# Kernel optimization log

Hardware: AMD Instinct MI355X
Metric: run time of the kernel (lower is better)

Reference implementation:

```python
import jax, jax.numpy as jnp
import numpy as np

B, T, C = 2, 4096, 768
H = 12
D = C // H  # head_dim = 64
SCALE = np.sqrt(D).astype(np.float32)


def setup_inputs() -> dict:
    key = jax.random.key(0)
    ks = jax.random.split(key, 5)
    s = 0.02
    return {
        "x": jax.random.normal(ks[0], (B, T, C), dtype=jnp.float32),
        "Wqkv": jax.random.normal(ks[1], (C, 3 * C), dtype=jnp.float32) * s,
        "bqkv": jnp.zeros((3 * C,), dtype=jnp.float32),
        "Wout": jax.random.normal(ks[2], (C, C), dtype=jnp.float32) * s,
        "bout": jnp.zeros((C,), dtype=jnp.float32),
    }


def reference(x, Wqkv, bqkv, Wout, bout):
    Bx, Tx, Cx = x.shape
    qkv = x @ Wqkv + bqkv                                   # [B,T,3C]
    qkv = qkv.reshape(Bx, Tx, 3, H, D)
    q, k, v = [jnp.moveaxis(qkv[:, :, i], 2, 1) for i in range(3)]  # each [B,H,T,D]
    attn = jnp.einsum("bhqd,bhkd->bhqk", q, k) / SCALE      # [B,H,T,T]
    causal = jnp.tril(jnp.ones((Tx, Tx), dtype=bool))
    attn = jnp.where(causal, attn, jnp.float32(-jnp.inf))
    attn = jax.nn.softmax(attn, axis=-1)
    out = jnp.einsum("bhqk,bhkd->bhqd", attn, v)            # [B,H,T,D]
    out = jnp.moveaxis(out, 1, 2).reshape(Bx, Tx, Cx)       # [B,T,C]
    return out @ Wout + bout
```

## Files before the change

kernel.cpp:

```cpp
#include <hip/hip_runtime.h>
#include <hip/hip_bf16.h>

#define T_DIM 4096
#define H_N 12
#define D_H 64
#define C_DIM 768
#define B_N 2

typedef short bf16x8 __attribute__((ext_vector_type(8)));
typedef float f32x4 __attribute__((ext_vector_type(4)));

__device__ __forceinline__ short f2bf(float f) {
    union { float f; unsigned u; } x; x.f = f;
    unsigned r = x.u + 0x7fffu + ((x.u >> 16) & 1u);
    return (short)(r >> 16);
}
__device__ __forceinline__ unsigned pk2bf(float a, float b) {
    union { float f; unsigned u; } x, y; x.f = a; y.f = b;
    unsigned ua = x.u + 0x7fffu + ((x.u >> 16) & 1u);
    unsigned ub = y.u + 0x7fffu + ((y.u >> 16) & 1u);
    return (ua >> 16) | (ub & 0xffff0000u);
}
__device__ __forceinline__ unsigned pktrunc(float lo, float hi) {
    union { float f; unsigned u; } a, b; a.f = lo; b.f = hi;
    return __builtin_amdgcn_perm(b.u, a.u, 0x07060302u);
}
__device__ __forceinline__ float bf2f(short s) {
    union { unsigned u; float f; } x; x.u = ((unsigned)(unsigned short)s) << 16;
    return x.f;
}

__device__ __forceinline__ void async_copy16(const void* g, void* l) {
    __builtin_amdgcn_global_load_lds(
        (const __attribute__((address_space(1))) unsigned*)g,
        (__attribute__((address_space(3))) unsigned*)l, 16, 0, 0);
}

#define Q_SCALE 0.18033688011112042f

__global__ __launch_bounds__(256) void xconv_kernel(
    const float* __restrict__ x, short* __restrict__ xb)
{
    size_t i = ((size_t)blockIdx.x * 256 + threadIdx.x) * 8;
    float4 a = *(const float4*)(x + i);
    float4 b = *(const float4*)(x + i + 4);
    unsigned pk[4];
    pk[0] = pk2bf(a.x, a.y); pk[1] = pk2bf(a.z, a.w);
    pk[2] = pk2bf(b.x, b.y); pk[3] = pk2bf(b.z, b.w);
    *(uint4*)(xb + i) = *(uint4*)pk;
}

__global__ __launch_bounds__(256) void wtrans_kernel(
    const float* __restrict__ W, short* __restrict__ Wt, int K, int N)
{
    const int wave = threadIdx.x >> 6, lane = threadIdx.x & 63;
    const int n = blockIdx.x * 256 + wave * 64 + lane;
    const int k0 = blockIdx.y * 128;
    for (int k = k0; k < k0 + 128; k += 8) {
        unsigned pk[4];
#pragma unroll
        for (int j = 0; j < 4; ++j)
            pk[j] = pk2bf(W[(size_t)(k + 2 * j) * N + n],
                          W[(size_t)(k + 2 * j + 1) * N + n]);
        *(uint4*)(Wt + (size_t)n * K + k) = *(uint4*)pk;
    }
}

__global__ __launch_bounds__(256) void qkv_kernel(
    const short* __restrict__ xb, const short* __restrict__ Wb,
    const float* __restrict__ bias,
    short* __restrict__ Qo, short* __restrict__ Ko, short* __restrict__ Vto)
{
    __shared__ short As[128 * 32];
    __shared__ short Bs[128 * 32];
    __shared__ short Vs[64][136];

    const int tid  = threadIdx.x;
    const int wave = tid >> 6, lane = tid & 63;
    const int quad = lane >> 4, l16 = lane & 15;
    const int wm = wave >> 1, wn = wave & 1;
    const int m0 = blockIdx.y * 128, n0 = blockIdx.x * 128;
    const int lrow = lane >> 2, lcc = lane & 3;

    f32x4 acc[4][4];
#pragma unroll
    for (int i = 0; i < 4; ++i)
#pragma unroll
        for (int j = 0; j < 4; ++j) acc[i][j] = (f32x4){0.f, 0.f, 0.f, 0.f};

    for (int k0 = 0; k0 < 768; k0 += 32) {
        __syncthreads();
#pragma unroll
        for (int i = 0; i < 2; ++i) {
            const int sbase = wave * 128 + i * 64;
            const int row = wave * 32 + i * 16 + lrow;
            async_copy16(xb + (size_t)(m0 + row) * 768 + k0 + lcc * 8, &As[sbase * 8]);
            async_copy16(Wb + (size_t)(n0 + row) * 768 + k0 + lcc * 8, &Bs[sbase * 8]);
        }
        asm volatile("s_waitcnt vmcnt(0)" ::: "memory");
        __syncthreads();

        bf16x8 af[4], bfr[4];
#pragma unroll
        for (int t = 0; t < 4; ++t)
            af[t] = *(const bf16x8*)&As[(wm * 64 + t * 16 + l16) * 32 + quad * 8];
#pragma unroll
        for (int t = 0; t < 4; ++t)
            bfr[t] = *(const bf16x8*)&Bs[(wn * 64 + t * 16 + l16) * 32 + quad * 8];
#pragma unroll
        for (int mt = 0; mt < 4; ++mt)
#pragma unroll
            for (int nt = 0; nt < 4; ++nt)
                acc[mt][nt] = __builtin_amdgcn_mfma_f32_16x16x32_bf16(
                    af[mt], bfr[nt], acc[mt][nt], 0, 0, 0);
    }

    if (n0 < 1536) {
#pragma unroll
        for (int nt = 0; nt < 4; ++nt) {
            int n = n0 + wn * 64 + nt * 16 + l16;
            float bv = bias[n];
            int which = n >= 768;
            int cw = n - which * 768;
            int h = cw >> 6, d = cw & 63;
            float scale = which ? 1.0f : Q_SCALE;
            short* dst = which ? Ko : Qo;
#pragma unroll
            for (int mt = 0; mt < 4; ++mt) {
#pragma unroll
                for (int reg = 0; reg < 4; ++reg) {
                    int m = m0 + wm * 64 + mt * 16 + quad * 4 + reg;
                    int b = m >> 12, t = m & 4095;
                    dst[(size_t)((b * H_N + h) * T_DIM + t) * D_H + d] =
                        f2bf((acc[mt][nt][reg] + bv) * scale);
                }
            }
        }
    } else {
        const int b = m0 >> 12, t0 = m0 & 4095;
        for (int p = 0; p < 2; ++p) {
            if (wn == p) {
#pragma unroll
                for (int nt = 0; nt < 4; ++nt) {
                    int n = n0 + wn * 64 + nt * 16 + l16;
                    float bv = bias[n];
#pragma unroll
                    for (int mt = 0; mt < 4; ++mt)
#pragma unroll
                        for (int reg = 0; reg < 4; ++reg)
                            Vs[nt * 16 + l16][wm * 64 + mt * 16 + quad * 4 + reg] =
                                f2bf(acc[mt][nt][reg] + bv);
                }
            }
            __syncthreads();
            int hh = ((n0 - 1536) >> 6) + p;
#pragma unroll
            for (int cc = tid; cc < 512; cc += 256) {
                int d = cc >> 3, part = cc & 7;
                bf16x8 v0 = *(const bf16x8*)&Vs[d][part * 16];
                bf16x8 v1 = *(const bf16x8*)&Vs[d][part * 16 + 8];
                size_t dst = ((size_t)(b * H_N + hh) * D_H + d) * T_DIM + t0 + part * 16;
                *(bf16x8*)(Vto + dst) = v0;
                *(bf16x8*)(Vto + dst + 8) = v1;
            }
            __syncthreads();
        }
    }
}

__global__ __launch_bounds__(256) void attn_partial_kernel(
    const short* __restrict__ Q, const short* __restrict__ K,
    const short* __restrict__ Vt, short* __restrict__ Opart,
    float* __restrict__ Lbuf)
{
    __shared__ short KsT[2][4096];
    __shared__ short VsT[2][4096];
    __shared__ short Ps[4][32][76];

    const int tid  = threadIdx.x;
    const int wave = tid >> 6, lane = tid & 63;
    const int quad = lane >> 4, l16 = lane & 15;
    const int bh = blockIdx.y;
    const int rr = blockIdx.x;

    int qj, ci;
    if (rr < 12) { qj = 12 + rr; ci = 0; }
    else if (rr < 28) { int t = rr - 12; qj = 24 + (t >> 1); ci = t & 1; }
    else {
        int t = rr - 28;
        if (t < 8) { int g = t >> 1, b = t & 1; int m = 12 - g;
                     qj = b ? (11 + m) : (m - 1); }
        else { int tt = t - 8; int g = tt / 3, b = tt - 3 * g; int m = 8 - g;
               qj = (b == 0) ? (m - 1) : ((b == 1) ? (11 + m) : (23 + m)); }
        ci = qj / 12;
    }
    const int q0 = qj * 128;
    const int kvStart = ci * 1536;
    const int kvEnd = min(kvStart + 1536, q0 + 128);
    const int ntiles = (kvEnd - kvStart) >> 6;
    const int off = (qj < 12) ? qj : ((qj < 24) ? 12 + (qj - 12) * 2
                                               : 36 + (qj - 24) * 3);
    const int s = bh * 60 + off + ci;
    const size_t base = (size_t)bh * T_DIM * D_H;
    const int row0 = q0 + wave * 32;

    bf16x8 qf[2][2];
#pragma unroll
    for (int qt = 0; qt < 2; ++qt)
#pragma unroll
        for (int ks = 0; ks < 2; ++ks)
            qf[qt][ks] = *(const bf16x8*)(
                Q + base + (size_t)(row0 + qt * 16 + l16) * 64 + ks * 32 + quad * 8);

    bf16x8 ones;
#pragma unroll
    for (int j = 0; j < 8; ++j) ones[j] = (short)0x3F80;

    f32x4 oacc[2][4], lacc[2];
#pragma unroll
    for (int qt = 0; qt < 2; ++qt) {
        lacc[qt] = (f32x4){0.f, 0.f, 0.f, 0.f};
#pragma unroll
        for (int nt = 0; nt < 4; ++nt) oacc[qt][nt] = (f32x4){0.f, 0.f, 0.f, 0.f};
    }

    const int srow = (wave * 128 + lane) >> 3;
    const int scol0 = (lane & 7) ^ (srow & 7);
    const int srow1 = (wave * 128 + 64 + lane) >> 3;
    const int scol1 = (lane & 7) ^ (srow1 & 7);

    {
        const int kv0 = kvStart;
        async_copy16(K + base + (size_t)(kv0 + srow) * 64 + scol0 * 8,
                     &KsT[0][(wave * 128) * 8]);
        async_copy16(Vt + base + (size_t)srow * T_DIM + kv0 + scol0 * 8,
                     &VsT[0][(wave * 128) * 8]);
        async_copy16(K + base + (size_t)(kv0 + srow1) * 64 + scol1 * 8,
                     &KsT[0][(wave * 128 + 64) * 8]);
        async_copy16(Vt + base + (size_t)srow1 * T_DIM + kv0 + scol1 * 8,
                     &VsT[0][(wave * 128 + 64) * 8]);
    }

    int buf = 0;
    for (int it = 0; it < ntiles; ++it) {
        const int kv0 = kvStart + it * 64;

        asm volatile("s_waitcnt vmcnt(0)" ::: "memory");
        asm volatile("s_barrier" ::: "memory");

        if (it + 1 < ntiles) {
            const int kn = kv0 + 64;
            async_copy16(K + base + (size_t)(kn + srow) * 64 + scol0 * 8,
                         &KsT[buf ^ 1][(wave * 128) * 8]);
            async_copy16(Vt + base + (size_t)srow * T_DIM + kn + scol0 * 8,
                         &VsT[buf ^ 1][(wave * 128) * 8]);
            async_copy16(K + base + (size_t)(kn + srow1) * 64 + scol1 * 8,
                         &KsT[buf ^ 1][(wave * 128 + 64) * 8]);
            async_copy16(Vt + base + (size_t)srow1 * T_DIM + kn + scol1 * 8,
                         &VsT[buf ^ 1][(wave * 128 + 64) * 8]);
        }

        if (kv0 <= row0 + 31) {
            const short* Kb = &KsT[buf][0];
            const short* Vb = &VsT[buf][0];

            f32x4 sacc[4][2];
#pragma unroll
            for (int mt = 0; mt < 4; ++mt)
#pragma unroll
                for (int qt = 0; qt < 2; ++qt)
                    sacc[mt][qt] = (f32x4){0.f, 0.f, 0.f, 0.f};
#pragma unroll
            for (int mt = 0; mt < 4; ++mt) {
                int R = mt * 16 + l16;
#pragma unroll
                for (int ks = 0; ks < 2; ++ks) {
                    bf16x8 kf = *(const bf16x8*)&Kb[(R * 8 + ((ks * 4 + quad) ^ (R & 7))) * 8];
                    sacc[mt][0] = __builtin_amdgcn_mfma_f32_16x16x32_bf16(
                        kf, qf[0][ks], sacc[mt][0], 0, 0, 0);
                    sacc[mt][1] = __builtin_amdgcn_mfma_f32_16x16x32_bf16(
                        kf, qf[1][ks], sacc[mt][1], 0, 0, 0);
                }
            }

            if (kv0 + 63 > row0) {
#pragma unroll
                for (int qt = 0; qt < 2; ++qt) {
                    int qrow = row0 + qt * 16 + l16;
#pragma unroll
                    for (int mt = 0; mt < 4; ++mt)
#pragma unroll
                        for (int reg = 0; reg < 4; ++reg)
                            if (kv0 + mt * 16 + quad * 4 + reg > qrow)
                                sacc[mt][qt][reg] = -1e30f;
                }
            }

#pragma unroll
            for (int qt = 0; qt < 2; ++qt) {
#pragma unroll
                for (int mt = 0; mt < 4; ++mt) {
                    float p0 = exp2f(sacc[mt][qt][0]);
                    float p1 = exp2f(sacc[mt][qt][1]);
                    float p2 = exp2f(sacc[mt][qt][2]);
                    float p3 = exp2f(sacc[mt][qt][3]);
                    uint2 pk;
                    pk.x = pktrunc(p0, p1);
                    pk.y = pktrunc(p2, p3);
                    *(uint2*)&Ps[wave][qt * 16 + l16][mt * 16 + quad * 4] = pk;
                }
            }

            asm volatile("s_waitcnt lgkmcnt(0)" ::: "memory");

#pragma unroll
            for (int ks = 0; ks < 2; ++ks) {
                bf16x8 pa0 = *(const bf16x8*)&Ps[wave][l16][ks * 32 + quad * 8];
                bf16x8 pa1 = *(const bf16x8*)&Ps[wave][16 + l16][ks * 32 + quad * 8];
                lacc[0] = __builtin_amdgcn_mfma_f32_16x16x32_bf16(pa0, ones, lacc[0], 0, 0, 0);
                lacc[1] = __builtin_amdgcn_mfma_f32_16x16x32_bf16(pa1, ones, lacc[1], 0, 0, 0);
#pragma unroll
                for (int nt = 0; nt < 4; ++nt) {
                    int R = nt * 16 + l16;
                    bf16x8 vf = *(const bf16x8*)&Vb[(R * 8 + ((ks * 4 + quad) ^ (R & 7))) * 8];
                    oacc[0][nt] = __builtin_amdgcn_mfma_f32_16x16x32_bf16(
                        pa0, vf, oacc[0][nt], 0, 0, 0);
                    oacc[1][nt] = __builtin_amdgcn_mfma_f32_16x16x32_bf16(
                        pa1, vf, oacc[1][nt], 0, 0, 0);
                }
            }
        }
        buf ^= 1;
    }

    short* op = Opart + (size_t)s * 8192;
#pragma unroll
    for (int qt = 0; qt < 2; ++qt)
#pragma unroll
        for (int nt = 0; nt < 4; ++nt)
#pragma unroll
            for (int reg = 0; reg < 4; ++reg) {
                int row = wave * 32 + qt * 16 + quad * 4 + reg;
                op[row * 64 + nt * 16 + l16] = f2bf(oacc[qt][nt][reg]);
            }
    if (l16 == 0) {
#pragma unroll
        for (int qt = 0; qt < 2; ++qt)
#pragma unroll
            for (int reg = 0; reg < 4; ++reg)
                Lbuf[s * 128 + wave * 32 + qt * 16 + quad * 4 + reg] = lacc[qt][reg];
    }
}

__global__ __launch_bounds__(256) void combine_kernel(
    const short* __restrict__ Opart, const float* __restrict__ Lbuf,
    short* __restrict__ O)
{
    const int tid = threadIdx.x;
    const int qi = blockIdx.x, bh = blockIdx.y;
    const int b = bh / H_N, h = bh - b * H_N;
    const int r = tid >> 2, cg = (tid & 3) * 16;
    const int qj = qi >> 1;
    const int riu = (qi & 1) * 64 + r;
    const int off = (qj < 12) ? qj : ((qj < 24) ? 12 + (qj - 12) * 2
                                               : 36 + (qj - 24) * 3);
    const int nc = qj / 12 + 1;
    const int s0 = bh * 60 + off;

    float l = 0.f;
    float res[16];
#pragma unroll
    for (int j = 0; j < 16; ++j) res[j] = 0.f;

    for (int ci = 0; ci < nc; ++ci) {
        const int su = s0 + ci;
        l += Lbuf[su * 128 + riu];
        const short* p = Opart + (size_t)su * 8192 + riu * 64 + cg;
        bf16x8 a0 = *(const bf16x8*)p;
        bf16x8 a1 = *(const bf16x8*)(p + 8);
#pragma unroll
        for (int j = 0; j < 8; ++j) { res[j] += bf2f(a0[j]); res[8 + j] += bf2f(a1[j]); }
    }

    float inv = 1.0f / l;
    unsigned pk[8];
#pragma unroll
    for (int j = 0; j < 8; ++j) pk[j] = pk2bf(res[2 * j] * inv, res[2 * j + 1] * inv);
    size_t o = ((size_t)b * T_DIM + qi * 64 + r) * C_DIM + h * 64 + cg;
    *(uint4*)(O + o)     = *(uint4*)&pk[0];
    *(uint4*)(O + o + 8) = *(uint4*)&pk[4];
}

__global__ __launch_bounds__(256) void out_kernel(
    const short* __restrict__ A, const short* __restrict__ Wb,
    const float* __restrict__ bias, float* __restrict__ out)
{
    __shared__ short As[128 * 32];
    __shared__ short Bs[128 * 32];

    const int tid  = threadIdx.x;
    const int wave = tid >> 6, lane = tid & 63;
    const int quad = lane >> 4, l16 = lane & 15;
    const int wm = wave >> 1, wn = wave & 1;
    const int m0 = blockIdx.y * 128, n0 = blockIdx.x * 128;
    const int lrow = lane >> 2, lcc = lane & 3;

    f32x4 acc[4][4];
#pragma unroll
    for (int i = 0; i < 4; ++i)
#pragma unroll
        for (int j = 0; j < 4; ++j) acc[i][j] = (f32x4){0.f, 0.f, 0.f, 0.f};

    for (int k0 = 0; k0 < 768; k0 += 32) {
        __syncthreads();
#pragma unroll
        for (int i = 0; i < 2; ++i) {
            const int sbase = wave * 128 + i * 64;
            const int row = wave * 32 + i * 16 + lrow;
            async_copy16(A  + (size_t)(m0 + row) * 768 + k0 + lcc * 8, &As[sbase * 8]);
            async_copy16(Wb + (size_t)(n0 + row) * 768 + k0 + lcc * 8, &Bs[sbase * 8]);
        }
        asm volatile("s_waitcnt vmcnt(0)" ::: "memory");
        __syncthreads();

        bf16x8 af[4], bfr[4];
#pragma unroll
        for (int t = 0; t < 4; ++t)
            af[t] = *(const bf16x8*)&As[(wm * 64 + t * 16 + l16) * 32 + quad * 8];
#pragma unroll
        for (int t = 0; t < 4; ++t)
            bfr[t] = *(const bf16x8*)&Bs[(wn * 64 + t * 16 + l16) * 32 + quad * 8];
#pragma unroll
        for (int mt = 0; mt < 4; ++mt)
#pragma unroll
            for (int nt = 0; nt < 4; ++nt)
                acc[mt][nt] = __builtin_amdgcn_mfma_f32_16x16x32_bf16(
                    af[mt], bfr[nt], acc[mt][nt], 0, 0, 0);
    }

#pragma unroll
    for (int nt = 0; nt < 4; ++nt) {
        int n = n0 + wn * 64 + nt * 16 + l16;
        float bv = bias[n];
#pragma unroll
        for (int mt = 0; mt < 4; ++mt) {
#pragma unroll
            for (int reg = 0; reg < 4; ++reg) {
                int m = m0 + wm * 64 + mt * 16 + quad * 4 + reg;
                out[(size_t)m * 768 + n] = acc[mt][nt][reg] + bv;
            }
        }
    }
}

extern "C" void kernel_launch(void* const* d_in, const int* in_sizes, int n_in,
                              void* d_out, int out_size, void* d_ws, size_t ws_size,
                              hipStream_t stream) {
    const float* x    = (const float*)d_in[0];
    const float* Wqkv = (const float*)d_in[1];
    const float* bqkv = (const float*)d_in[2];
    const float* Wout = (const float*)d_in[3];
    const float* bout = (const float*)d_in[4];
    float* out = (float*)d_out;

    const size_t per = (size_t)B_N * H_N * T_DIM * D_H;
    short* Q      = (short*)d_ws;
    short* K      = Q + per;
    short* Vt     = K + per;
    short* Woutb  = Vt + per;
    short* xb     = Woutb + (size_t)768 * 768;
    short* Wqkvb  = xb + per;
    short* Opart  = xb;
    float* Lbuf   = (float*)(Opart + (size_t)1440 * 8192);
    short* O      = Q;

    xconv_kernel<<<dim3(3072), 256, 0, stream>>>(x, xb);
    wtrans_kernel<<<dim3(9, 6), 256, 0, stream>>>(Wqkv, Wqkvb, 768, 2304);
    wtrans_kernel<<<dim3(3, 6), 256, 0, stream>>>(Wout, Woutb, 768, 768);
    qkv_kernel<<<dim3(18, 64), 256, 0, stream>>>(xb, Wqkvb, bqkv, Q, K, Vt);
    attn_partial_kernel<<<dim3(60, 24), 256, 0, stream>>>(Q, K, Vt, Opart, Lbuf);
    combine_kernel<<<dim3(64, 24), 256, 0, stream>>>(Opart, Lbuf, O);
    out_kernel<<<dim3(6, 64), 256, 0, stream>>>(O, Woutb, bout, out);
}
```

Baseline: 335.1 us.

## Load K/V fragments directly from global memory per wave, dropping LDS staging

The attention partial kernel no longer stages K and V tiles in double-buffered shared memory with async copies and block barriers. Each wave now reads its MFMA K and V fragments straight from global memory (relying on L1/L2 caching) and runs only over its own causal range, which removes the block-wide syncs. Shared memory use drops to the P buffer, and a launch-bounds occupancy hint of 4 is added. The cost is four waves re-reading the same K/V from cache with no cross-wave reuse in LDS, plus exposed global-load latency without software prefetch.

Result: slower. 426.8 us (+27.3%).

```diff
diff --git a/kernel.cpp b/kernel.cpp
--- a/kernel.cpp
+++ b/kernel.cpp
@@ -168,13 +168,11 @@
     }
 }
 
-__global__ __launch_bounds__(256) void attn_partial_kernel(
+__global__ __launch_bounds__(256, 4) void attn_partial_kernel(
     const short* __restrict__ Q, const short* __restrict__ K,
     const short* __restrict__ Vt, short* __restrict__ Opart,
     float* __restrict__ Lbuf)
 {
-    __shared__ short KsT[2][4096];
-    __shared__ short VsT[2][4096];
     __shared__ short Ps[4][32][76];
 
     const int tid  = threadIdx.x;
@@ -197,13 +195,15 @@
     const int q0 = qj * 128;
     const int kvStart = ci * 1536;
     const int kvEnd = min(kvStart + 1536, q0 + 128);
-    const int ntiles = (kvEnd - kvStart) >> 6;
     const int off = (qj < 12) ? qj : ((qj < 24) ? 12 + (qj - 12) * 2
                                                : 36 + (qj - 24) * 3);
     const int s = bh * 60 + off + ci;
     const size_t base = (size_t)bh * T_DIM * D_H;
     const int row0 = q0 + wave * 32;
 
+    const int kvEndW = min(kvEnd, row0 + 32);
+    const int ntw = (kvEndW - kvStart + 63) >> 6;
+
     bf16x8 qf[2][2];
 #pragma unroll
     for (int qt = 0; qt < 2; ++qt)
@@ -224,113 +224,82 @@
         for (int nt = 0; nt < 4; ++nt) oacc[qt][nt] = (f32x4){0.f, 0.f, 0.f, 0.f};
     }
 
-    const int srow = (wave * 128 + lane) >> 3;
-    const int scol0 = (lane & 7) ^ (srow & 7);
-    const int srow1 = (wave * 128 + 64 + lane) >> 3;
-    const int scol1 = (lane & 7) ^ (srow1 & 7);
-
-    {
-        const int kv0 = kvStart;
-        async_copy16(K + base + (size_t)(kv0 + srow) * 64 + scol0 * 8,
-                     &KsT[0][(wave * 128) * 8]);
-        async_copy16(Vt + base + (size_t)srow * T_DIM + kv0 + scol0 * 8,
-                     &VsT[0][(wave * 128) * 8]);
-        async_copy16(K + base + (size_t)(kv0 + srow1) * 64 + scol1 * 8,
-                     &KsT[0][(wave * 128 + 64) * 8]);
-        async_copy16(Vt + base + (size_t)srow1 * T_DIM + kv0 + scol1 * 8,
-                     &VsT[0][(wave * 128 + 64) * 8]);
-    }
-
-    int buf = 0;
-    for (int it = 0; it < ntiles; ++it) {
+    const short* Kp = K  + base + (size_t)l16 * 64    + quad * 8;
+    const short* Vp = Vt + base + (size_t)l16 * T_DIM + quad * 8;
+
+    for (int it = 0; it < ntw; ++it) {
         const int kv0 = kvStart + it * 64;
 
-        asm volatile("s_waitcnt vmcnt(0)" ::: "memory");
-        asm volatile("s_barrier" ::: "memory");
-
-        if (it + 1 < ntiles) {
-            const int kn = kv0 + 64;
-            async_copy16(K + base + (size_t)(kn + srow) * 64 + scol0 * 8,
-                         &KsT[buf ^ 1][(wave * 128) * 8]);
-            async_copy16(Vt + base + (size_t)srow * T_DIM + kn + scol0 * 8,
-                         &VsT[buf ^ 1][(wave * 128) * 8]);
-            async_copy16(K + base + (size_t)(kn + srow1) * 64 + scol1 * 8,
-                         &KsT[buf ^ 1][(wave * 128 + 64) * 8]);
-            async_copy16(Vt + base + (size_t)srow1 * T_DIM + kn + scol1 * 8,
-                         &VsT[buf ^ 1][(wave * 128 + 64) * 8]);
-        }
-
-        if (kv0 <= row0 + 31) {
-            const short* Kb = &KsT[buf][0];
-            const short* Vb = &VsT[buf][0];
-
-            f32x4 sacc[4][2];
-#pragma unroll
-            for (int mt = 0; mt < 4; ++mt)
-#pragma unroll
-                for (int qt = 0; qt < 2; ++qt)
-                    sacc[mt][qt] = (f32x4){0.f, 0.f, 0.f, 0.f};
+        f32x4 sacc[4][2];
+#pragma unroll
+        for (int mt = 0; mt < 4; ++mt)
+#pragma unroll
+            for (int qt = 0; qt < 2; ++qt)
+                sacc[mt][qt] = (f32x4){0.f, 0.f, 0.f, 0.f};
+#pragma unroll
+        for (int mt = 0; mt < 4; ++mt) {
+#pragma unroll
+            for (int ks = 0; ks < 2; ++ks) {
+                bf16x8 kf = *(const bf16x8*)(Kp + (size_t)(kv0 + mt * 16) * 64 + ks * 32);
+                sacc[mt][0] = __builtin_amdgcn_mfma_f32_16x16x32_bf16(
+                    kf, qf[0][ks], sacc[mt][0], 0, 0, 0);
+                sacc[mt][1] = __builtin_amdgcn_mfma_f32_16x16x32_bf16(
+                    kf, qf[1][ks], sacc[mt][1], 0, 0, 0);
+            }
+        }
+
+        if (kv0 + 63 > row0) {
+#pragma unroll
+            for (int qt = 0; qt < 2; ++qt) {
+                int qrow = row0 + qt * 16 + l16;
+#pragma unroll
+                for (int mt = 0; mt < 4; ++mt)
+#pragma unroll
+                    for (int reg = 0; reg < 4; ++reg)
+                        if (kv0 + mt * 16 + quad * 4 + reg > qrow)
+                            sacc[mt][qt][reg] = -1e30f;
+            }
+        }
+
+#pragma unroll
+        for (int qt = 0; qt < 2; ++qt) {
 #pragma unroll
             for (int mt = 0; mt < 4; ++mt) {
-                int R = mt * 16 + l16;
-#pragma unroll
-                for (int ks = 0; ks < 2; ++ks) {
-                    bf16x8 kf = *(const bf16x8*)&Kb[(R * 8 + ((ks * 4 + quad) ^ (R & 7))) * 8];
-                    sacc[mt][0] = __builtin_amdgcn_mfma_f32_16x16x32_bf16(
-                        kf, qf[0][ks], sacc[mt][0], 0, 0, 0);
-                    sacc[mt][1] = __builtin_amdgcn_mfma_f32_16x16x32_bf16(
-                        kf, qf[1][ks], sacc[mt][1], 0, 0, 0);
-                }
-            }
-
-            if (kv0 + 63 > row0) {
-#pragma unroll
-                for (int qt = 0; qt < 2; ++qt) {
-                    int qrow = row0 + qt * 16 + l16;
-#pragma unroll
-                    for (int mt = 0; mt < 4; ++mt)
-#pragma unroll
-                        for (int reg = 0; reg < 4; ++reg)
-                            if (kv0 + mt * 16 + quad * 4 + reg > qrow)
-                                sacc[mt][qt][reg] = -1e30f;
-                }
-            }
-
-#pragma unroll
-            for (int qt = 0; qt < 2; ++qt) {
-#pragma unroll
-                for (int mt = 0; mt < 4; ++mt) {
-                    float p0 = exp2f(sacc[mt][qt][0]);
-                    float p1 = exp2f(sacc[mt][qt][1]);
-                    float p2 = exp2f(sacc[mt][qt][2]);
-                    float p3 = exp2f(sacc[mt][qt][3]);
-                    uint2 pk;
-                    pk.x = pktrunc(p0, p1);
-                    pk.y = pktrunc(p2, p3);
-                    *(uint2*)&Ps[wave][qt * 16 + l16][mt * 16 + quad * 4] = pk;
-                }
-            }
-
-            asm volatile("s_waitcnt lgkmcnt(0)" ::: "memory");
-
-#pragma unroll
-            for (int ks = 0; ks < 2; ++ks) {
-                bf16x8 pa0 = *(const bf16x8*)&Ps[wave][l16][ks * 32 + quad * 8];
-                bf16x8 pa1 = *(const bf16x8*)&Ps[wave][16 + l16][ks * 32 + quad * 8];
-                lacc[0] = __builtin_amdgcn_mfma_f32_16x16x32_bf16(pa0, ones, lacc[0], 0, 0, 0);
-                lacc[1] = __builtin_amdgcn_mfma_f32_16x16x32_bf16(pa1, ones, lacc[1], 0, 0, 0);
-#pragma unroll
-                for (int nt = 0; nt < 4; ++nt) {
-                    int R = nt * 16 + l16;
-                    bf16x8 vf = *(const bf16x8*)&Vb[(R * 8 + ((ks * 4 + quad) ^ (R & 7))) * 8];
-                    oacc[0][nt] = __builtin_amdgcn_mfma_f32_16x16x32_bf16(
-                        pa0, vf, oacc[0][nt], 0, 0, 0);
-                    oacc[1][nt] = __builtin_amdgcn_mfma_f32_16x16x32_bf16(
-                        pa1, vf, oacc[1][nt], 0, 0, 0);
-                }
-            }
-        }
-        buf ^= 1;
+                float p0 = exp2f(sacc[mt][qt][0]);
+                float p1 = exp2f(sacc[mt][qt][1]);
+                float p2 = exp2f(sacc[mt][qt][2]);
+                float p3 = exp2f(sacc[mt][qt][3]);
+                uint2 pk;
+                pk.x = pktrunc(p0, p1);
+                pk.y = pktrunc(p2, p3);
+                *(uint2*)&Ps[wave][qt * 16 + l16][mt * 16 + quad * 4] = pk;
+            }
+        }
+
+        bf16x8 vf[2][4];
+#pragma unroll
+        for (int ks = 0; ks < 2; ++ks)
+#pragma unroll
+            for (int nt = 0; nt < 4; ++nt)
+                vf[ks][nt] = *(const bf16x8*)(
+                    Vp + (size_t)nt * 16 * T_DIM + kv0 + ks * 32);
+
+        asm volatile("s_waitcnt lgkmcnt(0)" ::: "memory");
+
+#pragma unroll
+        for (int ks = 0; ks < 2; ++ks) {
+            bf16x8 pa0 = *(const bf16x8*)&Ps[wave][l16][ks * 32 + quad * 8];
+            bf16x8 pa1 = *(const bf16x8*)&Ps[wave][16 + l16][ks * 32 + quad * 8];
+            lacc[0] = __builtin_amdgcn_mfma_f32_16x16x32_bf16(pa0, ones, lacc[0], 0, 0, 0);
+            lacc[1] = __builtin_amdgcn_mfma_f32_16x16x32_bf16(pa1, ones, lacc[1], 0, 0, 0);
+#pragma unroll
+            for (int nt = 0; nt < 4; ++nt) {
+                oacc[0][nt] = __builtin_amdgcn_mfma_f32_16x16x32_bf16(
+                    pa0, vf[ks][nt], oacc[0][nt], 0, 0, 0);
+                oacc[1][nt] = __builtin_amdgcn_mfma_f32_16x16x32_bf16(
+                    pa1, vf[ks][nt], oacc[1][nt], 0, 0, 0);
+            }
+        }
     }
 
     short* op = Opart + (size_t)s * 8192;
```

## Switch attention to 32x32x16 MFMA and keep P in registers via permlane32 swap

Applied to the files above, without the earlier changes.

Rewrites the attention partial kernel's inner loop to use 32x32x16 bf16 MFMA tiles instead of 16x16x32. The probability tile is remapped from the S accumulator layout to the A-operand layout with v_permlane32_swap, so the per-wave LDS staging buffer and its write/wait/read round trip go away. It also processes KV in 32-wide sub-tiles, skipping fully masked ones, and adds an occupancy hint of 4 blocks per CU. The risks are higher register pressure from the 16-wide accumulators and correctness depending on the lane mapping of the swap.

Result: faster. 308.9 us (-7.8%).

```diff
diff --git a/kernel.cpp b/kernel.cpp
--- a/kernel.cpp
+++ b/kernel.cpp
@@ -9,6 +9,7 @@
 
 typedef short bf16x8 __attribute__((ext_vector_type(8)));
 typedef float f32x4 __attribute__((ext_vector_type(4)));
+typedef float f32x16 __attribute__((ext_vector_type(16)));
 
 __device__ __forceinline__ short f2bf(float f) {
     union { float f; unsigned u; } x; x.f = f;
@@ -168,18 +169,17 @@
     }
 }
 
-__global__ __launch_bounds__(256) void attn_partial_kernel(
+__global__ __launch_bounds__(256, 4) void attn_partial_kernel(
     const short* __restrict__ Q, const short* __restrict__ K,
     const short* __restrict__ Vt, short* __restrict__ Opart,
     float* __restrict__ Lbuf)
 {
     __shared__ short KsT[2][4096];
     __shared__ short VsT[2][4096];
-    __shared__ short Ps[4][32][76];
 
     const int tid  = threadIdx.x;
     const int wave = tid >> 6, lane = tid & 63;
-    const int quad = lane >> 4, l16 = lane & 15;
+    const int l32 = lane & 31, hi = lane >> 5;
     const int bh = blockIdx.y;
     const int rr = blockIdx.x;
 
@@ -203,26 +203,21 @@
     const int s = bh * 60 + off + ci;
     const size_t base = (size_t)bh * T_DIM * D_H;
     const int row0 = q0 + wave * 32;
-
-    bf16x8 qf[2][2];
-#pragma unroll
-    for (int qt = 0; qt < 2; ++qt)
-#pragma unroll
-        for (int ks = 0; ks < 2; ++ks)
-            qf[qt][ks] = *(const bf16x8*)(
-                Q + base + (size_t)(row0 + qt * 16 + l16) * 64 + ks * 32 + quad * 8);
+    const int qrow = row0 + l32;
+
+    bf16x8 qf[4];
+#pragma unroll
+    for (int dk = 0; dk < 4; ++dk)
+        qf[dk] = *(const bf16x8*)(
+            Q + base + (size_t)(row0 + l32) * 64 + dk * 16 + hi * 8);
 
     bf16x8 ones;
 #pragma unroll
     for (int j = 0; j < 8; ++j) ones[j] = (short)0x3F80;
 
-    f32x4 oacc[2][4], lacc[2];
-#pragma unroll
-    for (int qt = 0; qt < 2; ++qt) {
-        lacc[qt] = (f32x4){0.f, 0.f, 0.f, 0.f};
-#pragma unroll
-        for (int nt = 0; nt < 4; ++nt) oacc[qt][nt] = (f32x4){0.f, 0.f, 0.f, 0.f};
-    }
+    f32x16 oacc[2], lacc;
+#pragma unroll
+    for (int r = 0; r < 16; ++r) { oacc[0][r] = 0.f; oacc[1][r] = 0.f; lacc[r] = 0.f; }
 
     const int srow = (wave * 128 + lane) >> 3;
     const int scol0 = (lane & 7) ^ (srow & 7);
@@ -264,91 +259,77 @@
             const short* Kb = &KsT[buf][0];
             const short* Vb = &VsT[buf][0];
 
-            f32x4 sacc[4][2];
-#pragma unroll
-            for (int mt = 0; mt < 4; ++mt)
-#pragma unroll
-                for (int qt = 0; qt < 2; ++qt)
-                    sacc[mt][qt] = (f32x4){0.f, 0.f, 0.f, 0.f};
-#pragma unroll
-            for (int mt = 0; mt < 4; ++mt) {
-                int R = mt * 16 + l16;
-#pragma unroll
-                for (int ks = 0; ks < 2; ++ks) {
-                    bf16x8 kf = *(const bf16x8*)&Kb[(R * 8 + ((ks * 4 + quad) ^ (R & 7))) * 8];
-                    sacc[mt][0] = __builtin_amdgcn_mfma_f32_16x16x32_bf16(
-                        kf, qf[0][ks], sacc[mt][0], 0, 0, 0);
-                    sacc[mt][1] = __builtin_amdgcn_mfma_f32_16x16x32_bf16(
-                        kf, qf[1][ks], sacc[mt][1], 0, 0, 0);
+#pragma unroll
+            for (int sub = 0; sub < 2; ++sub) {
+                if (kv0 + sub * 32 > row0 + 31) continue;
+
+                f32x16 sacc;
+#pragma unroll
+                for (int r = 0; r < 16; ++r) sacc[r] = 0.f;
+#pragma unroll
+                for (int dk = 0; dk < 4; ++dk) {
+                    int R = sub * 32 + l32;
+                    bf16x8 kf = *(const bf16x8*)
+                        &Kb[(R * 8 + ((dk * 2 + hi) ^ (R & 7))) * 8];
+                    sacc = __builtin_amdgcn_mfma_f32_32x32x16_bf16(
+                        kf, qf[dk], sacc, 0, 0, 0);
+                }
+
+                if (kv0 + sub * 32 + 31 > row0) {
+#pragma unroll
+                    for (int r = 0; r < 16; ++r) {
+                        int kvg = kv0 + sub * 32 + (r & 3) + 8 * (r >> 2) + 4 * hi;
+                        if (kvg > qrow) sacc[r] = -1e30f;
+                    }
+                }
+
+                unsigned w[8];
+#pragma unroll
+                for (int r2 = 0; r2 < 8; ++r2)
+                    w[r2] = pktrunc(exp2f(sacc[2 * r2]), exp2f(sacc[2 * r2 + 1]));
+
+                asm volatile("v_permlane32_swap_b32 %0, %1" : "+v"(w[0]), "+v"(w[2]));
+                asm volatile("v_permlane32_swap_b32 %0, %1" : "+v"(w[1]), "+v"(w[3]));
+                asm volatile("v_permlane32_swap_b32 %0, %1" : "+v"(w[4]), "+v"(w[6]));
+                asm volatile("v_permlane32_swap_b32 %0, %1" : "+v"(w[5]), "+v"(w[7]));
+                union { unsigned u[4]; bf16x8 v; } af0, af1;
+                af0.u[0] = w[0]; af0.u[1] = w[1]; af0.u[2] = w[2]; af0.u[3] = w[3];
+                af1.u[0] = w[4]; af1.u[1] = w[5]; af1.u[2] = w[6]; af1.u[3] = w[7];
+
+                lacc = __builtin_amdgcn_mfma_f32_32x32x16_bf16(
+                    af0.v, ones, lacc, 0, 0, 0);
+                lacc = __builtin_amdgcn_mfma_f32_32x32x16_bf16(
+                    af1.v, ones, lacc, 0, 0, 0);
+
+#pragma unroll
+                for (int kh = 0; kh < 2; ++kh) {
+                    bf16x8 pa = kh ? af1.v : af0.v;
+#pragma unroll
+                    for (int dt = 0; dt < 2; ++dt) {
+                        int R = dt * 32 + l32;
+                        bf16x8 vf = *(const bf16x8*)
+                            &Vb[(R * 8 + ((sub * 4 + kh * 2 + hi) ^ (R & 7))) * 8];
+                        oacc[dt] = __builtin_amdgcn_mfma_f32_32x32x16_bf16(
+                            pa, vf, oacc[dt], 0, 0, 0);
+                    }
                 }
             }
-
-            if (kv0 + 63 > row0) {
-#pragma unroll
-                for (int qt = 0; qt < 2; ++qt) {
-                    int qrow = row0 + qt * 16 + l16;
-#pragma unroll
-                    for (int mt = 0; mt < 4; ++mt)
-#pragma unroll
-                        for (int reg = 0; reg < 4; ++reg)
-                            if (kv0 + mt * 16 + quad * 4 + reg > qrow)
-                                sacc[mt][qt][reg] = -1e30f;
-                }
-            }
-
-#pragma unroll
-            for (int qt = 0; qt < 2; ++qt) {
-#pragma unroll
-                for (int mt = 0; mt < 4; ++mt) {
-                    float p0 = exp2f(sacc[mt][qt][0]);
-                    float p1 = exp2f(sacc[mt][qt][1]);
-                    float p2 = exp2f(sacc[mt][qt][2]);
-                    float p3 = exp2f(sacc[mt][qt][3]);
-                    uint2 pk;
-                    pk.x = pktrunc(p0, p1);
-                    pk.y = pktrunc(p2, p3);
-                    *(uint2*)&Ps[wave][qt * 16 + l16][mt * 16 + quad * 4] = pk;
-                }
-            }
-
-            asm volatile("s_waitcnt lgkmcnt(0)" ::: "memory");
-
-#pragma unroll
-            for (int ks = 0; ks < 2; ++ks) {
-                bf16x8 pa0 = *(const bf16x8*)&Ps[wave][l16][ks * 32 + quad * 8];
-                bf16x8 pa1 = *(const bf16x8*)&Ps[wave][16 + l16][ks * 32 + quad * 8];
-                lacc[0] = __builtin_amdgcn_mfma_f32_16x16x32_bf16(pa0, ones, lacc[0], 0, 0, 0);
-                lacc[1] = __builtin_amdgcn_mfma_f32_16x16x32_bf16(pa1, ones, lacc[1], 0, 0, 0);
-#pragma unroll
-                for (int nt = 0; nt < 4; ++nt) {
-                    int R = nt * 16 + l16;
-                    bf16x8 vf = *(const bf16x8*)&Vb[(R * 8 + ((ks * 4 + quad) ^ (R & 7))) * 8];
-                    oacc[0][nt] = __builtin_amdgcn_mfma_f32_16x16x32_bf16(
-                        pa0, vf, oacc[0][nt], 0, 0, 0);
-                    oacc[1][nt] = __builtin_amdgcn_mfma_f32_16x16x32_bf16(
-                        pa1, vf, oacc[1][nt], 0, 0, 0);
-                }
-            }
         }
         buf ^= 1;
     }
 
     short* op = Opart + (size_t)s * 8192;
 #pragma unroll
-    for (int qt = 0; qt < 2; ++qt)
-#pragma unroll
-        for (int nt = 0; nt < 4; ++nt)
-#pragma unroll
-            for (int reg = 0; reg < 4; ++reg) {
-                int row = wave * 32 + qt * 16 + quad * 4 + reg;
-                op[row * 64 + nt * 16 + l16] = f2bf(oacc[qt][nt][reg]);
-            }
-    if (l16 == 0) {
-#pragma unroll
-        for (int qt = 0; qt < 2; ++qt)
-#pragma unroll
-            for (int reg = 0; reg < 4; ++reg)
-                Lbuf[s * 128 + wave * 32 + qt * 16 + quad * 4 + reg] = lacc[qt][reg];
+    for (int dt = 0; dt < 2; ++dt)
+#pragma unroll
+        for (int r = 0; r < 16; ++r) {
+            int qr = wave * 32 + (r & 3) + 8 * (r >> 2) + 4 * hi;
+            op[qr * 64 + dt * 32 + l32] = f2bf(oacc[dt][r]);
+        }
+    if (l32 == 0) {
+#pragma unroll
+        for (int r = 0; r < 16; ++r)
+            Lbuf[s * 128 + wave * 32 + (r & 3) + 8 * (r >> 2) + 4 * hi] = lacc[r];
     }
 }
 
```
